# Kernel optimization log

Hardware: AMD Instinct MI355X
Metric: run time of the kernel (lower is better)

Reference implementation:

```python
import jax, jax.numpy as jnp
import numpy as np

E = 8        # num_experts
TOP_K = 2
DIM = 1024
DFF = DIM // 4
T = 32768    # batch*seq tokens


def setup_inputs() -> dict:
    key = jax.random.key(0)
    ks = jax.random.split(key, 5)
    x = jax.random.normal(ks[0], (T, DIM), dtype=jnp.float32)
    router_w = jax.random.normal(ks[1], (E, DIM), dtype=jnp.float32) * 0.02
    w1 = jax.random.normal(ks[2], (E, DIM, DFF), dtype=jnp.float32) * 0.02
    w2 = jax.random.normal(ks[3], (E, DFF, DIM), dtype=jnp.float32) * 0.02
    w3 = jax.random.normal(ks[4], (E, DIM, DFF), dtype=jnp.float32) * 0.02
    return {"x": x, "router_w": router_w, "w1": w1, "w2": w2, "w3": w3}


def reference(x, router_w, w1, w2, w3):
    # ---- Router ----
    logits = x @ router_w.T                          # [T, E]
    scores = jax.nn.softmax(logits.astype(jnp.float32), axis=1)
    # expert_bias is zero at init and noise_scale=0 -> topk on raw scores
    _, sel = jax.lax.top_k(scores, TOP_K)            # [T, K] expert indices
    top_scores = jnp.take_along_axis(scores, sel, axis=-1)
    top_scores = top_scores / jnp.sum(top_scores, axis=-1, keepdims=True)

    flat_experts = sel.reshape(-1)                   # [T*K]
    sorted_idx = jnp.argsort(flat_experts)           # stable sort, expert-centric order
    scatter_idx = sorted_idx // TOP_K                # original token id per row
    num_tokens_per_expert = jnp.bincount(flat_experts, length=E).astype(jnp.int32)

    x_gathered = x[scatter_idx]                      # [T*K, DIM]
    scores_sorted = top_scores.reshape(-1)[sorted_idx]  # [T*K]

    # ---- GroupedExpert: grouped GEMM SwiGLU in bf16 ----
    xb = x_gathered.astype(jnp.bfloat16)
    x1 = jax.lax.ragged_dot(xb, w1.astype(jnp.bfloat16), num_tokens_per_expert)
    x3 = jax.lax.ragged_dot(xb, w3.astype(jnp.bfloat16), num_tokens_per_expert)
    h = jax.nn.silu(x1) * x3                         # [T*K, DFF] bf16
    expert_out = jax.lax.ragged_dot(h, w2.astype(jnp.bfloat16), num_tokens_per_expert)
    expert_out = expert_out.astype(x.dtype)          # [T*K, DIM]

    # ---- Combine: weighted scatter-add back to token positions ----
    out = jnp.zeros_like(x).at[scatter_idx].add(expert_out * scores_sorted[:, None])
    return out
```

## Files before the change

kernel.cpp:

```cpp
#include <hip/hip_runtime.h>
#include <cstdint>
#include <cstddef>
#include <math.h>

#define T_TOK 32768
#define DIM   1024
#define DFF   256
#define NE    8
#define NB    16
#define ROWS  (T_TOK * 2)
#define MAXROWS 66560
#define MAXTILES (MAXROWS / 64)

typedef unsigned short u16;
typedef __attribute__((ext_vector_type(8))) short v8s;
typedef __attribute__((ext_vector_type(4))) float v4f;

__device__ __forceinline__ u16 f2bf(float f) {
  union { float f; unsigned u; } v; v.f = f;
  return (u16)((v.u + 0x7FFFu + ((v.u >> 16) & 1u)) >> 16);
}
__device__ __forceinline__ float bf2f(u16 b) {
  union { unsigned u; float f; } v; v.u = ((unsigned)b) << 16; return v.f;
}

#define WS_W13  ((size_t)0)
#define WS_W2T  ((size_t)8388608)
#define WS_H    ((size_t)12582912)
#define WS_RTOK ((size_t)46661632)
#define WS_RWT  ((size_t)46927872)
#define WS_CNT  ((size_t)47194112)
#define WS_CUR  ((size_t)47194176)
#define WS_OFF  ((size_t)47194240)
#define WS_SEL  ((size_t)47194368)
#define WS_WTS  ((size_t)47456512)

__global__ __launch_bounds__(256) void k_pack13(const float* __restrict__ w1,
                                                const float* __restrict__ w3,
                                                u16* __restrict__ W13p) {
  __shared__ float s1[32][33];
  __shared__ float s3[32][33];
  int e = blockIdx.z, k0 = blockIdx.x * 32, j0w = blockIdx.y;
  int tx = threadIdx.x, ty = threadIdx.y;
  size_t wbase = (size_t)e * DIM * DFF;
#pragma unroll
  for (int r = 0; r < 4; ++r) {
    int kl = ty + 8 * r;
    size_t src = wbase + (size_t)(k0 + kl) * DFF + j0w * 32 + tx;
    s1[kl][tx] = w1[src];
    s3[kl][tx] = w3[src];
  }
  __syncthreads();
  size_t obase = (size_t)e * 512 * 1024;
#pragma unroll
  for (int r = 0; r < 4; ++r) {
    int jl = ty + 8 * r;
    int n1 = 64 * j0w + jl;
    W13p[obase + (size_t)n1 * 1024 + k0 + tx]        = f2bf(s1[tx][jl]);
    W13p[obase + (size_t)(n1 + 32) * 1024 + k0 + tx] = f2bf(s3[tx][jl]);
  }
}

__global__ __launch_bounds__(256) void k_pack2(const float* __restrict__ w2,
                                               u16* __restrict__ W2t) {
  __shared__ float s[32][33];
  int e = blockIdx.z, k0 = blockIdx.x * 32, n0 = blockIdx.y * 32;
  int tx = threadIdx.x, ty = threadIdx.y;
#pragma unroll
  for (int r = 0; r < 4; ++r) {
    int kl = ty + 8 * r;
    s[kl][tx] = w2[(size_t)e * DFF * DIM + (size_t)(k0 + kl) * DIM + n0 + tx];
  }
  __syncthreads();
#pragma unroll
  for (int r = 0; r < 4; ++r) {
    int nl = ty + 8 * r;
    W2t[(size_t)e * DIM * DFF + (size_t)(n0 + nl) * DFF + k0 + tx] = f2bf(s[tx][nl]);
  }
}

__global__ __launch_bounds__(256) void k_router(const float* __restrict__ x,
                                                const float* __restrict__ rw,
                                                int* __restrict__ sel,
                                                float* __restrict__ wts,
                                                int* __restrict__ cnt) {
  __shared__ __align__(16) float s_rw[NE][1028];
  __shared__ __align__(16) float s_x[32][132];
  __shared__ float s_lg[256];
  __shared__ int s_cnt[NB];
  int tid = threadIdx.x;
  if (tid < NB) s_cnt[tid] = 0;
  {
    const float4* rw4 = (const float4*)rw;
#pragma unroll
    for (int r = 0; r < 8; ++r)
      *(float4*)(&s_rw[r][tid * 4]) = rw4[r * 256 + tid];
  }
  int tl = tid >> 3, e = tid & 7;
  float acc = 0.0f;
  const float4* x4 = (const float4*)x;
  for (int c = 0; c < 8; ++c) {
    __syncthreads();
#pragma unroll
    for (int j = 0; j < 4; ++j) {
      int slot = j * 256 + tid;
      int t = slot >> 5, kk = (slot & 31) * 4;
      *(float4*)(&s_x[t][kk]) = x4[((size_t)blockIdx.x * 32 + t) * 256 + c * 32 + (slot & 31)];
    }
    __syncthreads();
    const float* xp = &s_x[tl][0];
    const float* wp = &s_rw[e][c * 128];
#pragma unroll 16
    for (int k = 0; k < 128; ++k) acc = fmaf(xp[k], wp[k], acc);
  }
  s_lg[tid] = acc;
  __syncthreads();
  if ((tid & 7) == 0) {
    int t = blockIdx.x * 32 + tl;
    const float* lg = s_lg + tid;
    int b0 = 0; float v0 = lg[0];
#pragma unroll
    for (int ee = 1; ee < NE; ++ee) if (lg[ee] > v0) { v0 = lg[ee]; b0 = ee; }
    int b1 = -1; float v1 = -1e30f;
#pragma unroll
    for (int ee = 0; ee < NE; ++ee) if (ee != b0 && lg[ee] > v1) { v1 = lg[ee]; b1 = ee; }
    float w0 = 1.0f / (1.0f + expf(v1 - v0));
    sel[2 * t] = b0; sel[2 * t + 1] = b1;
    wts[2 * t] = w0; wts[2 * t + 1] = 1.0f - w0;
    atomicAdd(&s_cnt[2 * b0], 1);
    atomicAdd(&s_cnt[2 * b1 + 1], 1);
  }
  __syncthreads();
  if (tid < NB && s_cnt[tid]) atomicAdd(&cnt[tid], s_cnt[tid]);
}

__global__ void k_scan(const int* __restrict__ cnt, int* __restrict__ offs) {
  if (threadIdx.x == 0 && blockIdx.x == 0) {
    int o = 0;
#pragma unroll
    for (int b = 0; b < NB; ++b) { offs[b] = o; o += (cnt[b] + 63) & ~63; }
    offs[NB] = o;
  }
}

__global__ __launch_bounds__(256) void k_scatter(const int* __restrict__ sel,
                                                 const float* __restrict__ wts,
                                                 const int* __restrict__ offs,
                                                 int* __restrict__ cursor,
                                                 int* __restrict__ rtok,
                                                 float* __restrict__ rwt) {
  __shared__ int s_cnt[NB], s_base[NB];
  int tid = threadIdx.x;
  if (tid < NB) s_cnt[tid] = 0;
  __syncthreads();
  int g = blockIdx.x * 256 + tid;
  int b = sel[g] * 2 + (g & 1);
  int lpos = atomicAdd(&s_cnt[b], 1);
  __syncthreads();
  if (tid < NB) s_base[tid] = s_cnt[tid] ? atomicAdd(&cursor[tid], s_cnt[tid]) : 0;
  __syncthreads();
  int row = offs[b] + s_base[b] + lpos;
  rtok[row] = g >> 1;
  rwt[row] = wts[g];
}

__global__ __launch_bounds__(512, 4) void k_gemm1(const float* __restrict__ x,
                                                  const u16* __restrict__ W13p,
                                                  const int* __restrict__ rtok,
                                                  const int* __restrict__ offs,
                                                  u16* __restrict__ h) {
  __shared__ __align__(16) u16 A_s[64][40];
  __shared__ __align__(16) u16 B_s[512][40];
  int row0 = blockIdx.x * 64;
  if (row0 >= offs[NB]) return;
  int b2 = 0;
  while (row0 >= offs[b2 + 1]) ++b2;
  int e = b2 >> 1;
  int tid = threadIdx.x;
  int ar = tid >> 3, ac = (tid & 7) * 4;
  int tk = rtok[row0 + ar];
  if (tk < 0) tk = 0;
  const float* xrow = x + (size_t)tk * DIM;
  const u16* Bb = W13p + (size_t)e * 512 * 1024;
  int wv = tid >> 6, lane = tid & 63;
  int lr = lane & 15, q = lane >> 4;
  v4f acc[4][4] = {};
  for (int k0 = 0; k0 < DIM; k0 += 32) {
    float4 xv = *(const float4*)(xrow + k0 + ac);
    ushort4 a4;
    a4.x = f2bf(xv.x); a4.y = f2bf(xv.y); a4.z = f2bf(xv.z); a4.w = f2bf(xv.w);
    *(ushort4*)(&A_s[ar][ac]) = a4;
#pragma unroll
    for (int qq = 0; qq < 4; ++qq) {
      int id = qq * 512 + tid;
      int n = id >> 2, c8 = (id & 3) * 8;
      *(uint4*)(&B_s[n][c8]) = *(const uint4*)(Bb + (size_t)n * 1024 + k0 + c8);
    }
    __syncthreads();
    v8s a[4], b[4];
#pragma unroll
    for (int mt = 0; mt < 4; ++mt) a[mt] = *(const v8s*)(&A_s[16 * mt + lr][q * 8]);
#pragma unroll
    for (int nt = 0; nt < 4; ++nt) b[nt] = *(const v8s*)(&B_s[64 * wv + 16 * nt + lr][q * 8]);
#pragma unroll
    for (int mt = 0; mt < 4; ++mt)
#pragma unroll
      for (int nt = 0; nt < 4; ++nt)
        acc[mt][nt] = __builtin_amdgcn_mfma_f32_16x16x32_bf16(a[mt], b[nt], acc[mt][nt], 0, 0, 0);
    __syncthreads();
  }
#pragma unroll
  for (int mt = 0; mt < 4; ++mt)
#pragma unroll
    for (int nt = 0; nt < 2; ++nt)
#pragma unroll
      for (int r = 0; r < 4; ++r) {
        float x1 = bf2f(f2bf(acc[mt][nt][r]));
        float x3 = bf2f(f2bf(acc[mt][nt + 2][r]));
        float hv = x1 * x3 / (1.0f + __expf(-x1));
        int row = row0 + 16 * mt + q * 4 + r;
        int col = 32 * wv + 16 * nt + lr;
        h[(size_t)row * DFF + col] = f2bf(hv);
      }
}

__global__ __launch_bounds__(512, 4) void k_gemm2(const u16* __restrict__ h,
                                                  const u16* __restrict__ W2t,
                                                  const int* __restrict__ rtok,
                                                  const float* __restrict__ rwt,
                                                  const int* __restrict__ offs,
                                                  float* __restrict__ out,
                                                  int pass) {
  __shared__ __align__(16) u16 A_s[64][40];
  __shared__ __align__(16) u16 B_s[512][40];
  __shared__ int s_tok[64];
  __shared__ float s_wt[64];
  int row0 = blockIdx.x * 64;
  if (row0 >= offs[NB]) return;
  int b2 = 0;
  while (row0 >= offs[b2 + 1]) ++b2;
  if ((b2 & 1) != pass) return;
  int e = b2 >> 1;
  int nb = blockIdx.y;
  int tid = threadIdx.x;
  if (tid < 64) { s_tok[tid] = rtok[row0 + tid]; s_wt[tid] = rwt[row0 + tid]; }
  int ar = tid >> 3, ac = (tid & 7) * 4;
  const u16* hrow = h + (size_t)(row0 + ar) * DFF;
  const u16* Bb = W2t + (size_t)e * DIM * DFF + (size_t)nb * 512 * DFF;
  int wv = tid >> 6, lane = tid & 63;
  int lr = lane & 15, q = lane >> 4;
  v4f acc[4][4] = {};
  for (int k0 = 0; k0 < DFF; k0 += 32) {
    *(ushort4*)(&A_s[ar][ac]) = *(const ushort4*)(hrow + k0 + ac);
#pragma unroll
    for (int qq = 0; qq < 4; ++qq) {
      int id = qq * 512 + tid;
      int n = id >> 2, c8 = (id & 3) * 8;
      *(uint4*)(&B_s[n][c8]) = *(const uint4*)(Bb + (size_t)n * DFF + k0 + c8);
    }
    __syncthreads();
    v8s a[4], b[4];
#pragma unroll
    for (int mt = 0; mt < 4; ++mt) a[mt] = *(const v8s*)(&A_s[16 * mt + lr][q * 8]);
#pragma unroll
    for (int nt = 0; nt < 4; ++nt) b[nt] = *(const v8s*)(&B_s[64 * wv + 16 * nt + lr][q * 8]);
#pragma unroll
    for (int mt = 0; mt < 4; ++mt)
#pragma unroll
      for (int nt = 0; nt < 4; ++nt)
        acc[mt][nt] = __builtin_amdgcn_mfma_f32_16x16x32_bf16(a[mt], b[nt], acc[mt][nt], 0, 0, 0);
    __syncthreads();
  }
#pragma unroll
  for (int mt = 0; mt < 4; ++mt)
#pragma unroll
    for (int nt = 0; nt < 4; ++nt) {
      int col = nb * 512 + 64 * wv + 16 * nt + lr;
#pragma unroll
      for (int r = 0; r < 4; ++r) {
        int m = 16 * mt + q * 4 + r;
        int tok = s_tok[m];
        if (tok < 0) continue;
        float val = bf2f(f2bf(acc[mt][nt][r])) * s_wt[m];
        float* p = out + (size_t)tok * DIM + col;
        if (pass == 0) *p = val;
        else           *p += val;
      }
    }
}

extern "C" void kernel_launch(void* const* d_in, const int* in_sizes, int n_in,
                              void* d_out, int out_size, void* d_ws, size_t ws_size,
                              hipStream_t stream) {
  (void)in_sizes; (void)n_in; (void)ws_size; (void)out_size;
  const float* x  = (const float*)d_in[0];
  const float* rw = (const float*)d_in[1];
  const float* w1 = (const float*)d_in[2];
  const float* w2 = (const float*)d_in[3];
  const float* w3 = (const float*)d_in[4];
  float* out = (float*)d_out;
  char* ws = (char*)d_ws;
  u16*   W13p = (u16*)(ws + WS_W13);
  u16*   W2t  = (u16*)(ws + WS_W2T);
  u16*   hbuf = (u16*)(ws + WS_H);
  int*   rtok = (int*)(ws + WS_RTOK);
  float* rwt  = (float*)(ws + WS_RWT);
  int*   cnt  = (int*)(ws + WS_CNT);
  int*   cur  = (int*)(ws + WS_CUR);
  int*   offs = (int*)(ws + WS_OFF);
  int*   sel  = (int*)(ws + WS_SEL);
  float* wts  = (float*)(ws + WS_WTS);

  hipMemsetAsync(ws + WS_RTOK, 0xFF, (size_t)MAXROWS * 4, stream);
  hipMemsetAsync(ws + WS_CNT, 0, 128, stream);

  k_pack13<<<dim3(32, 8, 8), dim3(32, 8), 0, stream>>>(w1, w3, W13p);
  k_pack2 <<<dim3(8, 32, 8), dim3(32, 8), 0, stream>>>(w2, W2t);
  k_router<<<dim3(T_TOK / 32), dim3(256), 0, stream>>>(x, rw, sel, wts, cnt);
  k_scan  <<<dim3(1), dim3(64), 0, stream>>>(cnt, offs);
  k_scatter<<<dim3(ROWS / 256), dim3(256), 0, stream>>>(sel, wts, offs, cur, rtok, rwt);
  k_gemm1 <<<dim3(MAXTILES), dim3(512), 0, stream>>>(x, W13p, rtok, offs, hbuf);
  k_gemm2 <<<dim3(MAXTILES, 2), dim3(512), 0, stream>>>(hbuf, W2t, rtok, rwt, offs, out, 0);
  k_gemm2 <<<dim3(MAXTILES, 2), dim3(512), 0, stream>>>(hbuf, W2t, rtok, rwt, offs, out, 1);
}
```

Measured before the change: 601.9 us.

## Write GEMM2 output to row buffer and combine per token in a separate kernel

GEMM2 used to run twice with a slot-parity filter and scattered fp32 stores (and read-modify-write adds) straight into token positions. Now it runs once, stages each tile through LDS and writes coalesced bf16 rows into a 128MB intermediate buffer. A new combine kernel reads each token's two expert rows through a position map, applies the routing weights and writes fp32 output in one coalesced pass. This trades extra intermediate traffic for fewer launches and no scattered writes.

```diff
diff --git a/kernel.cpp b/kernel.cpp
--- a/kernel.cpp
+++ b/kernel.cpp
@@ -27,13 +27,14 @@
 #define WS_W13  ((size_t)0)
 #define WS_W2T  ((size_t)8388608)
 #define WS_H    ((size_t)12582912)
-#define WS_RTOK ((size_t)46661632)
-#define WS_RWT  ((size_t)46927872)
-#define WS_CNT  ((size_t)47194112)
-#define WS_CUR  ((size_t)47194176)
-#define WS_OFF  ((size_t)47194240)
-#define WS_SEL  ((size_t)47194368)
-#define WS_WTS  ((size_t)47456512)
+#define WS_Y    ((size_t)46661632)
+#define WS_RTOK ((size_t)182976512)
+#define WS_POS  ((size_t)183242752)
+#define WS_CNT  ((size_t)183504896)
+#define WS_CUR  ((size_t)183504960)
+#define WS_OFF  ((size_t)183505024)
+#define WS_SEL  ((size_t)183505152)
+#define WS_WTS  ((size_t)183767296)
 
 __global__ __launch_bounds__(256) void k_pack13(const float* __restrict__ w1,
                                                 const float* __restrict__ w3,
@@ -144,11 +145,10 @@
 }
 
 __global__ __launch_bounds__(256) void k_scatter(const int* __restrict__ sel,
-                                                 const float* __restrict__ wts,
                                                  const int* __restrict__ offs,
                                                  int* __restrict__ cursor,
                                                  int* __restrict__ rtok,
-                                                 float* __restrict__ rwt) {
+                                                 int* __restrict__ pos) {
   __shared__ int s_cnt[NB], s_base[NB];
   int tid = threadIdx.x;
   if (tid < NB) s_cnt[tid] = 0;
@@ -161,7 +161,7 @@
   __syncthreads();
   int row = offs[b] + s_base[b] + lpos;
   rtok[row] = g >> 1;
-  rwt[row] = wts[g];
+  pos[g] = row;
 }
 
 __global__ __launch_bounds__(512, 4) void k_gemm1(const float* __restrict__ x,
@@ -226,24 +226,17 @@
 
 __global__ __launch_bounds__(512, 4) void k_gemm2(const u16* __restrict__ h,
                                                   const u16* __restrict__ W2t,
-                                                  const int* __restrict__ rtok,
-                                                  const float* __restrict__ rwt,
                                                   const int* __restrict__ offs,
-                                                  float* __restrict__ out,
-                                                  int pass) {
+                                                  u16* __restrict__ y) {
   __shared__ __align__(16) u16 A_s[64][40];
   __shared__ __align__(16) u16 B_s[512][40];
-  __shared__ int s_tok[64];
-  __shared__ float s_wt[64];
   int row0 = blockIdx.x * 64;
   if (row0 >= offs[NB]) return;
   int b2 = 0;
   while (row0 >= offs[b2 + 1]) ++b2;
-  if ((b2 & 1) != pass) return;
   int e = b2 >> 1;
   int nb = blockIdx.y;
   int tid = threadIdx.x;
-  if (tid < 64) { s_tok[tid] = rtok[row0 + tid]; s_wt[tid] = rwt[row0 + tid]; }
   int ar = tid >> 3, ac = (tid & 7) * 4;
   const u16* hrow = h + (size_t)(row0 + ar) * DFF;
   const u16* Bb = W2t + (size_t)e * DIM * DFF + (size_t)nb * 512 * DFF;
@@ -271,22 +264,49 @@
         acc[mt][nt] = __builtin_amdgcn_mfma_f32_16x16x32_bf16(a[mt], b[nt], acc[mt][nt], 0, 0, 0);
     __syncthreads();
   }
-#pragma unroll
-  for (int mt = 0; mt < 4; ++mt)
-#pragma unroll
-    for (int nt = 0; nt < 4; ++nt) {
-      int col = nb * 512 + 64 * wv + 16 * nt + lr;
-#pragma unroll
-      for (int r = 0; r < 4; ++r) {
-        int m = 16 * mt + q * 4 + r;
-        int tok = s_tok[m];
-        if (tok < 0) continue;
-        float val = bf2f(f2bf(acc[mt][nt][r])) * s_wt[m];
-        float* p = out + (size_t)tok * DIM + col;
-        if (pass == 0) *p = val;
-        else           *p += val;
-      }
+  u16* Ts = &B_s[0][0];
+#pragma unroll
+  for (int mt = 0; mt < 4; ++mt) {
+#pragma unroll
+    for (int nt = 0; nt < 4; ++nt)
+#pragma unroll
+      for (int r = 0; r < 4; ++r)
+        Ts[(q * 4 + r) * 520 + 64 * wv + 16 * nt + lr] = f2bf(acc[mt][nt][r]);
+    __syncthreads();
+#pragma unroll
+    for (int i = 0; i < 2; ++i) {
+      int j = tid + 512 * i;
+      int rr = j >> 6, cc = j & 63;
+      uint4 v = *(const uint4*)(Ts + rr * 520 + cc * 8);
+      *(uint4*)(y + (size_t)(row0 + 16 * mt + rr) * 1024 + nb * 512 + cc * 8) = v;
     }
+    __syncthreads();
+  }
+}
+
+__global__ __launch_bounds__(256) void k_combine(const u16* __restrict__ y,
+                                                 const int* __restrict__ pos,
+                                                 const float* __restrict__ wts,
+                                                 float* __restrict__ out) {
+  int tid = threadIdx.x, wv = tid >> 6, lane = tid & 63;
+  int t = blockIdx.x * 4 + wv;
+  int r0 = pos[2 * t], r1 = pos[2 * t + 1];
+  float w0 = wts[2 * t], w1 = wts[2 * t + 1];
+  const uint4* y0 = (const uint4*)(y + (size_t)r0 * 1024);
+  const uint4* y1 = (const uint4*)(y + (size_t)r1 * 1024);
+  float* o = out + (size_t)t * 1024;
+#pragma unroll
+  for (int i = 0; i < 2; ++i) {
+    int j = lane + 64 * i;
+    uint4 a = y0[j], b = y1[j];
+    const u16* pa = (const u16*)&a;
+    const u16* pb = (const u16*)&b;
+    float f[8];
+#pragma unroll
+    for (int k = 0; k < 8; ++k) f[k] = bf2f(pa[k]) * w0 + bf2f(pb[k]) * w1;
+    *(float4*)(o + j * 8)     = *(float4*)&f[0];
+    *(float4*)(o + j * 8 + 4) = *(float4*)&f[4];
+  }
 }
 
 extern "C" void kernel_launch(void* const* d_in, const int* in_sizes, int n_in,
@@ -303,8 +323,9 @@
   u16*   W13p = (u16*)(ws + WS_W13);
   u16*   W2t  = (u16*)(ws + WS_W2T);
   u16*   hbuf = (u16*)(ws + WS_H);
+  u16*   ybuf = (u16*)(ws + WS_Y);
   int*   rtok = (int*)(ws + WS_RTOK);
-  float* rwt  = (float*)(ws + WS_RWT);
+  int*   pos  = (int*)(ws + WS_POS);
   int*   cnt  = (int*)(ws + WS_CNT);
   int*   cur  = (int*)(ws + WS_CUR);
   int*   offs = (int*)(ws + WS_OFF);
@@ -318,8 +339,8 @@
   k_pack2 <<<dim3(8, 32, 8), dim3(32, 8), 0, stream>>>(w2, W2t);
   k_router<<<dim3(T_TOK / 32), dim3(256), 0, stream>>>(x, rw, sel, wts, cnt);
   k_scan  <<<dim3(1), dim3(64), 0, stream>>>(cnt, offs);
-  k_scatter<<<dim3(ROWS / 256), dim3(256), 0, stream>>>(sel, wts, offs, cur, rtok, rwt);
+  k_scatter<<<dim3(ROWS / 256), dim3(256), 0, stream>>>(sel, offs, cur, rtok, pos);
   k_gemm1 <<<dim3(MAXTILES), dim3(512), 0, stream>>>(x, W13p, rtok, offs, hbuf);
-  k_gemm2 <<<dim3(MAXTILES, 2), dim3(512), 0, stream>>>(hbuf, W2t, rtok, rwt, offs, out, 0);
-  k_gemm2 <<<dim3(MAXTILES, 2), dim3(512), 0, stream>>>(hbuf, W2t, rtok, rwt, offs, out, 1);
-}
+  k_gemm2 <<<dim3(MAXTILES, 2), dim3(512), 0, stream>>>(hbuf, W2t, offs, ybuf);
+  k_combine<<<dim3(T_TOK / 4), dim3(256), 0, stream>>>(ybuf, pos, wts, out);
+}
```

Measured after the change: 523.0 us. 1.15x faster.
